# Kernel tuning notes

Hardware: AMD Instinct MI355X
Metric: run time of the kernel (lower is better)

Reference implementation:

```python
import jax, jax.numpy as jnp
import numpy as np

B, S, E, H = 4, 2048, 1024, 16
HD = E // H  # 64 head dim


def setup_inputs() -> dict:
    key = jax.random.key(0)
    ks = jax.random.split(key, 6)
    x = jax.random.normal(ks[0], (B, S, E), dtype=jnp.float32)
    mask = jax.random.randint(ks[1], (B, S, S), 0, 2, dtype=jnp.int32)
    # per-head qkv Linear(E -> 3*HD), stacked over heads: weight [H, 3*HD, E]
    lim = 1.0 / np.sqrt(E)
    Wqkv = jax.random.uniform(ks[2], (H, 3 * HD, E), minval=-lim, maxval=lim, dtype=jnp.float32)
    bqkv = jax.random.uniform(ks[3], (H, 3 * HD), minval=-lim, maxval=lim, dtype=jnp.float32)
    Wo = jax.random.uniform(ks[4], (E, E), minval=-lim, maxval=lim, dtype=jnp.float32)
    bo = jax.random.uniform(ks[5], (E,), minval=-lim, maxval=lim, dtype=jnp.float32)
    return {"x": x, "mask": mask, "Wqkv": Wqkv, "bqkv": bqkv, "Wo": Wo, "bo": bo}


def reference(x, mask, Wqkv, bqkv, Wo, bo):
    # fused per-head qkv projection: [B,S,E] x [H,3HD,E] -> [B,H,S,3HD]
    qkv = jnp.einsum('bse,hfe->bhsf', x, Wqkv) + bqkv[None, :, None, :]
    q, k, v = jnp.split(qkv, 3, axis=-1)  # each [B,H,S,HD]
    scale = 1.0 / jnp.sqrt(jnp.float32(HD))
    scores = jnp.einsum('bhqd,bhkd->bhqk', q, k) * scale  # [B,H,S,S]
    # NOTE: original masked_fill sets masked scores to 0.0 (not -inf)
    scores = jnp.where(mask[:, None, :, :] == 1, 0.0, scores)
    attn = jax.nn.softmax(scores, axis=-1)
    ctx = jnp.einsum('bhqk,bhkd->bhqd', attn, v)  # [B,H,S,HD]
    ctx = ctx.transpose(0, 2, 1, 3).reshape(B, S, E)  # concat heads
    return ctx @ Wo.T + bo
```

## Files before the change

### kernel.cpp

```cpp
#include <hip/hip_runtime.h>
#include <stdint.h>

#define B_ 4
#define S_ 2048
#define E_ 1024
#define H_ 16
#define HD_ 64

typedef __attribute__((ext_vector_type(8))) short bf16x8;
typedef __attribute__((ext_vector_type(4))) float f32x4;

__device__ __forceinline__ ushort f2b(float f) {
    union { float f; uint32_t u; } c; c.f = f;
    return (ushort)((c.u + 0x8000u) >> 16);
}

__device__ __forceinline__ uint32_t pkbf_t(float a, float b) {
    union { float f; uint32_t u; } ca, cb; ca.f = a; cb.f = b;
#if __has_builtin(__builtin_amdgcn_perm)
    return __builtin_amdgcn_perm(cb.u, ca.u, 0x07060302u);
#else
    return (ca.u >> 16) | (cb.u & 0xFFFF0000u);
#endif
}

__device__ __forceinline__ uint32_t keepmask(uint32_t wn, int pos) {
#if __has_builtin(__builtin_amdgcn_sbfe)
    return (uint32_t)__builtin_amdgcn_sbfe((int)wn, pos, 1);
#else
    return (uint32_t)(((int32_t)(wn << (31 - pos))) >> 31);
#endif
}

#if __has_builtin(__builtin_amdgcn_exp2f)
#define EXP2(x) __builtin_amdgcn_exp2f(x)
#else
#define EXP2(x) exp2f(x)
#endif

__device__ __forceinline__ void gl2lds16(const ushort* g, const ushort* l) {
    __builtin_amdgcn_global_load_lds(
        (const __attribute__((address_space(1))) unsigned int*)g,
        (__attribute__((address_space(3))) unsigned int*)l,
        16, 0, 0);
}

__global__ __launch_bounds__(256) void cvt_all(
    const float* __restrict__ x, const float* __restrict__ wq, const float* __restrict__ wo,
    ushort* __restrict__ xb, ushort* __restrict__ wqb, ushort* __restrict__ wob) {
    int i = blockIdx.x * 256 + threadIdx.x;
    const float* src; ushort* dst; int off;
    if (i < 2097152)      { src = x;  dst = xb;  off = i; }
    else if (i < 2883584) { src = wq; dst = wqb; off = i - 2097152; }
    else                  { src = wo; dst = wob; off = i - 2883584; }
    float4 f = ((const float4*)src)[off];
    ushort4 o;
    o.x = f2b(f.x); o.y = f2b(f.y); o.z = f2b(f.z); o.w = f2b(f.w);
    ((ushort4*)dst)[off] = o;
}

__global__ __launch_bounds__(256) void pack_mask(const int* __restrict__ mask,
                                                 uint32_t* __restrict__ mb) {
    int i = blockIdx.x * 256 + threadIdx.x;
    unsigned long long bal = __ballot(mask[i] == 1);
    int lane = threadIdx.x & 63;
    if (lane < 2) {
        int b = i >> 22, q = (i >> 11) & 2047, c = i & 2047;
        int kt = c >> 6;
        mb[((uint64_t)(b * 32 + kt) * 2048 + q) * 2 + lane] =
            (lane == 0) ? (uint32_t)bal : (uint32_t)(bal >> 32);
    }
}

template <int KD>
__device__ __forceinline__ void gemm_bt_core(
    const ushort* __restrict__ A, const ushort* __restrict__ Bm,
    int m0, int n0, ushort* L, f32x4 (&acc)[4][4])
{
    constexpr int NST = KD / 32;
    const int tid  = threadIdx.x;
    const int lane = tid & 63;
    const int wave = tid >> 6;
    const int wm = wave >> 1, wn = wave & 1;
    const int fr = lane & 15;
    const int fk = (lane >> 4) * 8;
    const int lrow = lane >> 2;
    const int lk   = (lane & 3) * 8;

    const f32x4 fz = {0.f, 0.f, 0.f, 0.f};
#pragma unroll
    for (int i = 0; i < 4; ++i)
#pragma unroll
        for (int j = 0; j < 4; ++j) acc[i][j] = fz;

    ushort* s0 = L;
    ushort* s1 = L + 8192;
    ushort* s2 = L + 16384;

    const uint64_t arow = (uint64_t)(m0 + lrow) * KD + lk;
    const uint64_t brow = (uint64_t)(n0 + lrow) * KD + lk;

#define GEMM_STAGE(k0, slot)                                                     \
    {                                                                            \
        _Pragma("unroll")                                                        \
        for (int t = 0; t < 2; ++t) {                                            \
            const int r0 = t * 64 + wave * 16;                                   \
            gl2lds16(&A [arow + (uint64_t)r0 * KD + (k0)], &(slot)[r0 * 32]);    \
            gl2lds16(&Bm[brow + (uint64_t)r0 * KD + (k0)], &(slot)[4096 + r0 * 32]); \
        }                                                                        \
    }

    GEMM_STAGE(0, s0);
    GEMM_STAGE(32, s1);
    asm volatile("s_waitcnt vmcnt(4)" ::: "memory");
    __builtin_amdgcn_s_barrier();
    __builtin_amdgcn_sched_barrier(0);

    ushort* cur = s0; ushort* nxt = s1; ushort* tgt = s2;

    for (int kt = 0; kt < NST; ++kt) {
        if (kt < NST - 2) GEMM_STAGE((kt + 2) * 32, tgt);

        bf16x8 af[4], bfr[4];
#pragma unroll
        for (int i = 0; i < 4; ++i)
            af[i] = *(const bf16x8*)&cur[(wm * 64 + i * 16 + fr) * 32 + fk];
#pragma unroll
        for (int j = 0; j < 4; ++j)
            bfr[j] = *(const bf16x8*)&cur[4096 + (wn * 64 + j * 16 + fr) * 32 + fk];
        __builtin_amdgcn_s_setprio(1);
#pragma unroll
        for (int i = 0; i < 4; ++i)
#pragma unroll
            for (int j = 0; j < 4; ++j)
                acc[i][j] = __builtin_amdgcn_mfma_f32_16x16x32_bf16(af[i], bfr[j], acc[i][j], 0, 0, 0);
        __builtin_amdgcn_s_setprio(0);

        if (kt < NST - 2) {
            asm volatile("s_waitcnt vmcnt(4)" ::: "memory");
        } else {
            asm volatile("s_waitcnt vmcnt(0)" ::: "memory");
        }
        __builtin_amdgcn_s_barrier();
        __builtin_amdgcn_sched_barrier(0);

        ushort* o = cur; cur = nxt; nxt = tgt; tgt = o;
    }
#undef GEMM_STAGE
}

__global__ __launch_bounds__(256) void qkv_gemm(
    const ushort* __restrict__ xb, const ushort* __restrict__ wb,
    const float* __restrict__ bqkv,
    ushort* __restrict__ qo, ushort* __restrict__ ko, ushort* __restrict__ vto)
{
    __shared__ __align__(16) ushort L[24576];
    f32x4 acc[4][4];
    const int lin = blockIdx.x;
    const int swz = (lin & 7) * 192 + (lin >> 3);
    const int m0 = (swz & 63) * 128;
    const int n0 = (swz >> 6) * 128;
    gemm_bt_core<1024>(xb, wb, m0, n0, L, acc);

    const int lane = threadIdx.x & 63, wave = threadIdx.x >> 6;
    const int wm = wave >> 1, wn = wave & 1;
    const int col = lane & 15, rg = lane >> 4;
    const float QSC = 0.125f * 1.4426950408889634f;
#pragma unroll
    for (int j = 0; j < 4; ++j) {
        const int n = n0 + wn * 64 + j * 16 + col;
        const int h = n / 192, f = n % 192;
        const float bias = bqkv[n];
#pragma unroll
        for (int i2 = 0; i2 < 4; ++i2) {
            const int mbase = m0 + wm * 64 + i2 * 16 + rg * 4;
            if (f < 128) {
#pragma unroll
                for (int v = 0; v < 4; ++v) {
                    const int m = mbase + v;
                    const int b = m >> 11, s = m & 2047;
                    const float val = acc[i2][j][v] + bias;
                    if (f < 64) qo[((uint64_t)(b * 16 + h) * 2048 + s) * 64 + f]        = f2b(val * QSC);
                    else        ko[((uint64_t)(b * 16 + h) * 2048 + s) * 64 + (f - 64)] = f2b(val);
                }
            } else {
                const int b = mbase >> 11, s = mbase & 2047;
                ushort4 pk;
                pk.x = f2b(acc[i2][j][0] + bias);
                pk.y = f2b(acc[i2][j][1] + bias);
                pk.z = f2b(acc[i2][j][2] + bias);
                pk.w = f2b(acc[i2][j][3] + bias);
                *(ushort4*)&vto[((uint64_t)(b * 16 + h) * 64 + (f - 128)) * 2048 + s] = pk;
            }
        }
    }
}

__global__ __launch_bounds__(256, 3) void attn_kernel(
    const ushort* __restrict__ qa, const ushort* __restrict__ ka,
    const ushort* __restrict__ vta, const uint32_t* __restrict__ mbits,
    ushort* __restrict__ ctxo)
{
    __shared__ __align__(16) ushort LDSH[24576];
    ushort* const Ks0 = LDSH;
    ushort* const Vt0 = LDSH + 4096;
    ushort* const Ks1 = LDSH + 8192;
    ushort* const Vt1 = LDSH + 12288;
    ushort* const Ks2 = LDSH + 16384;
    ushort* const Vt2 = LDSH + 20480;
    ushort* const CTX = LDSH;

    const int bid = blockIdx.x;
    const int bh = (bid & 7) * 8 + (bid >> 7);
    const int qb = (bid >> 3) & 15;
    const int b = bh >> 4;
    const int tid = threadIdx.x, lane = tid & 63, wave = tid >> 6;
    const int col = lane & 15, rg = lane >> 4;

    const uint64_t bhoff = (uint64_t)bh * (S_ * 64);
    const ushort* qp = qa + bhoff + (uint64_t)qb * 128 * 64;
    const ushort* kp = ka + bhoff;
    const ushort* vp = vta + bhoff;
    const uint32_t* mk0 = mbits + ((uint64_t)(b * 32) * 2048 + qb * 128 + wave * 32 + col) * 2;
    const uint32_t* mk1 = mk0 + 32;

    const int lr = lane >> 3;
    const int usw = (lane & 7) ^ lr;
    const int r0s = wave * 16 + lr;
    const int r1s = r0s + 8;
    const int sg0 = (r0s & 32) | ((r0s & 12) << 1) | ((r0s & 16) >> 2) | (r0s & 3);
    const int sg1 = (r1s & 32) | ((r1s & 12) << 1) | ((r1s & 16) >> 2) | (r1s & 3);
    const int kb0 = sg0 * 64 + usw * 8;
    const int kb1 = sg1 * 64 + usw * 8;
    const int vb0 = r0s * 2048 + usw * 8;
    const int vb1 = r1s * 2048 + usw * 8;
    const int ldst0 = wave * 1024;
    const int ldst1 = ldst0 + 512;

    bf16x8 aq[2][2];
#pragma unroll
    for (int i = 0; i < 2; ++i)
#pragma unroll
        for (int k2 = 0; k2 < 2; ++k2)
            aq[i][k2] = *(const bf16x8*)&qp[(wave * 32 + i * 16 + col) * 64 + k2 * 32 + rg * 8];

    gl2lds16(&kp[kb0], &Ks0[ldst0]);
    gl2lds16(&kp[kb1], &Ks0[ldst1]);
    gl2lds16(&vp[vb0], &Vt0[ldst0]);
    gl2lds16(&vp[vb1], &Vt0[ldst1]);
    uint2 m_cur0 = *(const uint2*)mk0;
    uint2 m_cur1 = *(const uint2*)mk1;
    gl2lds16(&kp[4096 + kb0], &Ks1[ldst0]);
    gl2lds16(&kp[4096 + kb1], &Ks1[ldst1]);
    gl2lds16(&vp[vb0 + 64], &Vt1[ldst0]);
    gl2lds16(&vp[vb1 + 64], &Vt1[ldst1]);
    uint2 m_nxt0 = *(const uint2*)(mk0 + 4096);
    uint2 m_nxt1 = *(const uint2*)(mk1 + 4096);
    uint2 m_new0 = m_nxt0, m_new1 = m_nxt1;
    asm volatile("s_waitcnt vmcnt(0)" ::: "memory");
    __builtin_amdgcn_s_barrier();
    __builtin_amdgcn_sched_barrier(0);

    const f32x4 fz = {0.f, 0.f, 0.f, 0.f};
    f32x4 acc[4][2];
#pragma unroll
    for (int dt = 0; dt < 4; ++dt)
#pragma unroll
        for (int i = 0; i < 2; ++i) acc[dt][i] = fz;
    f32x4 acc5[2] = {fz, fz};

    bf16x8 vone;
#pragma unroll
    for (int e = 0; e < 8; ++e) vone[e] = (short)0x3F80;

    int bpos[2][4];
#pragma unroll
    for (int p = 0; p < 2; ++p)
#pragma unroll
        for (int v = 0; v < 4; ++v) bpos[p][v] = rg * 8 + p * 4 + v;

    const int u0 = (rg ^ (col & 7)) << 3;

    const ushort* cK = Ks0; const ushort* cV = Vt0;
    const ushort* nK = Ks1; const ushort* nV = Vt1;
    ushort* tK = Ks2; ushort* tV = Vt2;

    for (int kt = 0; kt < 32; ++kt) {
        if (kt < 30) {
            const int k2 = (kt + 2) * 4096;
            gl2lds16(&kp[k2 + kb0], &tK[ldst0]);
            gl2lds16(&kp[k2 + kb1], &tK[ldst1]);
            gl2lds16(&vp[vb0 + (kt + 2) * 64], &tV[ldst0]);
            gl2lds16(&vp[vb1 + (kt + 2) * 64], &tV[ldst1]);
            m_new0 = *(const uint2*)(mk0 + (uint64_t)(kt + 2) * 4096);
            m_new1 = *(const uint2*)(mk1 + (uint64_t)(kt + 2) * 4096);
        }

        f32x4 sc[2][4];
        __builtin_amdgcn_s_setprio(1);
#pragma unroll
        for (int j = 0; j < 4; ++j) {
            bf16x8 bk0 = *(const bf16x8*)&cK[(j * 16 + col) * 64 + u0];
            bf16x8 bk1 = *(const bf16x8*)&cK[(j * 16 + col) * 64 + (u0 ^ 32)];
#pragma unroll
            for (int i = 0; i < 2; ++i) {
                f32x4 z = __builtin_amdgcn_mfma_f32_16x16x32_bf16(bk0, aq[i][0], fz, 0, 0, 0);
                sc[i][j] = __builtin_amdgcn_mfma_f32_16x16x32_bf16(bk1, aq[i][1], z, 0, 0, 0);
            }
        }
        __builtin_amdgcn_s_setprio(0);

        bf16x8 bp[2][2];
#pragma unroll
        for (int i = 0; i < 2; ++i) {
            const uint2 mw = i ? m_cur1 : m_cur0;
            const uint32_t wnx = ~mw.x, wny = ~mw.y;
            union { uint32_t w[4]; bf16x8 v; } p0, p1;
#pragma unroll
            for (int j = 0; j < 4; ++j) {
                const uint32_t wn = (j & 2) ? wny : wnx;
                const int p = j & 1;
                float pe[4];
#pragma unroll
                for (int v = 0; v < 4; ++v) {
                    union { float f; uint32_t u; } cu;
                    cu.f = sc[i][j][v];
                    cu.u &= keepmask(wn, bpos[p][v]);
                    pe[v] = EXP2(cu.f);
                }
                const uint32_t lo = pkbf_t(pe[0], pe[1]);
                const uint32_t hi = pkbf_t(pe[2], pe[3]);
                if (j < 2) { p0.w[p * 2] = lo; p0.w[p * 2 + 1] = hi; }
                else       { p1.w[p * 2] = lo; p1.w[p * 2 + 1] = hi; }
            }
            bp[i][0] = p0.v;
            bp[i][1] = p1.v;
        }

        __builtin_amdgcn_s_setprio(1);
#pragma unroll
        for (int i = 0; i < 2; ++i) {
            acc5[i] = __builtin_amdgcn_mfma_f32_16x16x32_bf16(vone, bp[i][0], acc5[i], 0, 0, 0);
            acc5[i] = __builtin_amdgcn_mfma_f32_16x16x32_bf16(vone, bp[i][1], acc5[i], 0, 0, 0);
        }
#pragma unroll
        for (int dt = 0; dt < 4; ++dt) {
            bf16x8 av0 = *(const bf16x8*)&cV[(dt * 16 + col) * 64 + u0];
            bf16x8 av1 = *(const bf16x8*)&cV[(dt * 16 + col) * 64 + (u0 ^ 32)];
#pragma unroll
            for (int i = 0; i < 2; ++i) {
                acc[dt][i] = __builtin_amdgcn_mfma_f32_16x16x32_bf16(av0, bp[i][0], acc[dt][i], 0, 0, 0);
                acc[dt][i] = __builtin_amdgcn_mfma_f32_16x16x32_bf16(av1, bp[i][1], acc[dt][i], 0, 0, 0);
            }
        }
        __builtin_amdgcn_s_setprio(0);

        if (kt < 30) {
            asm volatile("s_waitcnt vmcnt(6)" ::: "memory");
        } else {
            asm volatile("s_waitcnt vmcnt(0)" ::: "memory");
        }
        __builtin_amdgcn_s_barrier();
        __builtin_amdgcn_sched_barrier(0);

        const ushort* oK = cK; const ushort* oV = cV;
        cK = nK; cV = nV; nK = tK; nV = tV; tK = (ushort*)oK; tV = (ushort*)oV;
        m_cur0 = m_nxt0; m_cur1 = m_nxt1; m_nxt0 = m_new0; m_nxt1 = m_new1;
    }

    float linv[2];
#pragma unroll
    for (int i = 0; i < 2; ++i) linv[i] = 1.0f / acc5[i][0];

#pragma unroll
    for (int dt = 0; dt < 4; ++dt)
#pragma unroll
        for (int i = 0; i < 2; ++i) {
            const int q = wave * 32 + i * 16 + col;
            const int d = dt * 16 + rg * 4;
            const int gg = (d >> 3) ^ (q & 7);
            ushort4 pk;
            pk.x = f2b(acc[dt][i][0] * linv[i]);
            pk.y = f2b(acc[dt][i][1] * linv[i]);
            pk.z = f2b(acc[dt][i][2] * linv[i]);
            pk.w = f2b(acc[dt][i][3] * linv[i]);
            *(ushort4*)&CTX[q * 64 + gg * 8 + (d & 7)] = pk;
        }
    __syncthreads();
    const int h = bh & 15;
    const uint64_t obase = (uint64_t)(b * S_ + qb * 128) * E_ + (uint64_t)h * 64;
#pragma unroll
    for (int t4 = 0; t4 < 4; ++t4) {
        const int id = tid + t4 * 256;
        const int r = id >> 3, c8 = id & 7;
        *(bf16x8*)&ctxo[obase + (uint64_t)r * E_ + c8 * 8] =
            *(const bf16x8*)&CTX[r * 64 + ((c8 ^ (r & 7)) << 3)];
    }
}

__global__ __launch_bounds__(256) void out_gemm(
    const ushort* __restrict__ ctxb, const ushort* __restrict__ wob,
    const float* __restrict__ bo, float* __restrict__ out)
{
    __shared__ __align__(16) ushort L[24576];
    f32x4 acc[4][4];
    const int lin = blockIdx.x;
    const int swz = (lin & 7) * 64 + (lin >> 3);
    const int m0 = (swz & 63) * 128;
    const int n0 = (swz >> 6) * 128;
    gemm_bt_core<1024>(ctxb, wob, m0, n0, L, acc);

    const int lane = threadIdx.x & 63, wave = threadIdx.x >> 6;
    const int wm = wave >> 1, wn = wave & 1;
    const int col = lane & 15, rg = lane >> 4;
#pragma unroll
    for (int j = 0; j < 4; ++j) {
        const int n = n0 + wn * 64 + j * 16 + col;
        const float bias = bo[n];
#pragma unroll
        for (int i2 = 0; i2 < 4; ++i2) {
            const int mb2 = m0 + wm * 64 + i2 * 16 + rg * 4;
#pragma unroll
            for (int v = 0; v < 4; ++v)
                out[(uint64_t)(mb2 + v) * 1024 + n] = acc[i2][j][v] + bias;
        }
    }
}

extern "C" void kernel_launch(void* const* d_in, const int* in_sizes, int n_in,
                              void* d_out, int out_size, void* d_ws, size_t ws_size,
                              hipStream_t stream)
{
    const float* x    = (const float*)d_in[0];
    const int*   mask = (const int*)d_in[1];
    const float* Wqkv = (const float*)d_in[2];
    const float* bqkv = (const float*)d_in[3];
    const float* Wo   = (const float*)d_in[4];
    const float* bo   = (const float*)d_in[5];
    float* out = (float*)d_out;

    char* p = (char*)d_ws;
    ushort* xb  = (ushort*)p; p += (size_t)8388608 * 2;
    ushort* wqb = (ushort*)p; p += (size_t)3145728 * 2;
    ushort* wob = (ushort*)p; p += (size_t)1048576 * 2;
    ushort* qo  = (ushort*)p; p += (size_t)8388608 * 2;
    ushort* ko  = (ushort*)p; p += (size_t)8388608 * 2;
    ushort* vto = (ushort*)p; p += (size_t)8388608 * 2;
    ushort* ctx = (ushort*)p; p += (size_t)8388608 * 2;
    uint32_t* mb = (uint32_t*)p;

    cvt_all<<<12288, 256, 0, stream>>>(x, Wqkv, Wo, xb, wqb, wob);
    pack_mask<<<65536, 256, 0, stream>>>(mask, mb);
    qkv_gemm<<<1536, 256, 0, stream>>>(xb, wqb, bqkv, qo, ko, vto);
    attn_kernel<<<1024, 256, 0, stream>>>(qo, ko, vto, mb, ctx);
    out_gemm<<<512, 256, 0, stream>>>(ctx, wob, bo, out);
}
```

Before: 353.3 us.

## Software-pipeline attention loop: overlap QK^T of next tile with softmax/PV

Restructures the attention inner loop so each phase computes QK^T scores for tile kt while running the mask/exp softmax and PV MFMAs for tile kt-1, using ping-pong score registers and a manual two-step unroll. The K/V tile issue moves after a barrier that follows the PV step, and the mask words are carried in a four-deep register rotation. The aim is to hide exp/VALU latency behind MFMA work and keep the matrix units busy. In exchange it raises register pressure, since two score sets are live at once, and adds an extra barrier per iteration.

```diff
diff --git a/kernel.cpp b/kernel.cpp
--- a/kernel.cpp
+++ b/kernel.cpp
@@ -244,19 +244,19 @@
         for (int k2 = 0; k2 < 2; ++k2)
             aq[i][k2] = *(const bf16x8*)&qp[(wave * 32 + i * 16 + col) * 64 + k2 * 32 + rg * 8];
 
+    uint2 m_a0 = *(const uint2*)mk0;
+    uint2 m_a1 = *(const uint2*)mk1;
+    uint2 m_b0 = *(const uint2*)(mk0 + 4096);
+    uint2 m_b1 = *(const uint2*)(mk1 + 4096);
+    uint2 m_c0, m_c1, m_d0, m_d1;
     gl2lds16(&kp[kb0], &Ks0[ldst0]);
     gl2lds16(&kp[kb1], &Ks0[ldst1]);
     gl2lds16(&vp[vb0], &Vt0[ldst0]);
     gl2lds16(&vp[vb1], &Vt0[ldst1]);
-    uint2 m_cur0 = *(const uint2*)mk0;
-    uint2 m_cur1 = *(const uint2*)mk1;
     gl2lds16(&kp[4096 + kb0], &Ks1[ldst0]);
     gl2lds16(&kp[4096 + kb1], &Ks1[ldst1]);
     gl2lds16(&vp[vb0 + 64], &Vt1[ldst0]);
     gl2lds16(&vp[vb1 + 64], &Vt1[ldst1]);
-    uint2 m_nxt0 = *(const uint2*)(mk0 + 4096);
-    uint2 m_nxt1 = *(const uint2*)(mk1 + 4096);
-    uint2 m_new0 = m_nxt0, m_new1 = m_nxt1;
     asm volatile("s_waitcnt vmcnt(0)" ::: "memory");
     __builtin_amdgcn_s_barrier();
     __builtin_amdgcn_sched_barrier(0);
@@ -281,92 +281,125 @@
 
     const int u0 = (rg ^ (col & 7)) << 3;
 
-    const ushort* cK = Ks0; const ushort* cV = Vt0;
-    const ushort* nK = Ks1; const ushort* nV = Vt1;
-    ushort* tK = Ks2; ushort* tV = Vt2;
-
-    for (int kt = 0; kt < 32; ++kt) {
-        if (kt < 30) {
-            const int k2 = (kt + 2) * 4096;
-            gl2lds16(&kp[k2 + kb0], &tK[ldst0]);
-            gl2lds16(&kp[k2 + kb1], &tK[ldst1]);
-            gl2lds16(&vp[vb0 + (kt + 2) * 64], &tV[ldst0]);
-            gl2lds16(&vp[vb1 + (kt + 2) * 64], &tV[ldst1]);
-            m_new0 = *(const uint2*)(mk0 + (uint64_t)(kt + 2) * 4096);
-            m_new1 = *(const uint2*)(mk1 + (uint64_t)(kt + 2) * 4096);
-        }
-
-        f32x4 sc[2][4];
-        __builtin_amdgcn_s_setprio(1);
-#pragma unroll
-        for (int j = 0; j < 4; ++j) {
-            bf16x8 bk0 = *(const bf16x8*)&cK[(j * 16 + col) * 64 + u0];
-            bf16x8 bk1 = *(const bf16x8*)&cK[(j * 16 + col) * 64 + (u0 ^ 32)];
-#pragma unroll
-            for (int i = 0; i < 2; ++i) {
-                f32x4 z = __builtin_amdgcn_mfma_f32_16x16x32_bf16(bk0, aq[i][0], fz, 0, 0, 0);
-                sc[i][j] = __builtin_amdgcn_mfma_f32_16x16x32_bf16(bk1, aq[i][1], z, 0, 0, 0);
-            }
-        }
-        __builtin_amdgcn_s_setprio(0);
-
-        bf16x8 bp[2][2];
-#pragma unroll
-        for (int i = 0; i < 2; ++i) {
-            const uint2 mw = i ? m_cur1 : m_cur0;
-            const uint32_t wnx = ~mw.x, wny = ~mw.y;
-            union { uint32_t w[4]; bf16x8 v; } p0, p1;
-#pragma unroll
-            for (int j = 0; j < 4; ++j) {
-                const uint32_t wn = (j & 2) ? wny : wnx;
-                const int p = j & 1;
-                float pe[4];
-#pragma unroll
-                for (int v = 0; v < 4; ++v) {
-                    union { float f; uint32_t u; } cu;
-                    cu.f = sc[i][j][v];
-                    cu.u &= keepmask(wn, bpos[p][v]);
-                    pe[v] = EXP2(cu.f);
-                }
-                const uint32_t lo = pkbf_t(pe[0], pe[1]);
-                const uint32_t hi = pkbf_t(pe[2], pe[3]);
-                if (j < 2) { p0.w[p * 2] = lo; p0.w[p * 2 + 1] = hi; }
-                else       { p1.w[p * 2] = lo; p1.w[p * 2 + 1] = hi; }
-            }
-            bp[i][0] = p0.v;
-            bp[i][1] = p1.v;
-        }
-
-        __builtin_amdgcn_s_setprio(1);
-#pragma unroll
-        for (int i = 0; i < 2; ++i) {
-            acc5[i] = __builtin_amdgcn_mfma_f32_16x16x32_bf16(vone, bp[i][0], acc5[i], 0, 0, 0);
-            acc5[i] = __builtin_amdgcn_mfma_f32_16x16x32_bf16(vone, bp[i][1], acc5[i], 0, 0, 0);
-        }
-#pragma unroll
-        for (int dt = 0; dt < 4; ++dt) {
-            bf16x8 av0 = *(const bf16x8*)&cV[(dt * 16 + col) * 64 + u0];
-            bf16x8 av1 = *(const bf16x8*)&cV[(dt * 16 + col) * 64 + (u0 ^ 32)];
-#pragma unroll
-            for (int i = 0; i < 2; ++i) {
-                acc[dt][i] = __builtin_amdgcn_mfma_f32_16x16x32_bf16(av0, bp[i][0], acc[dt][i], 0, 0, 0);
-                acc[dt][i] = __builtin_amdgcn_mfma_f32_16x16x32_bf16(av1, bp[i][1], acc[dt][i], 0, 0, 0);
-            }
-        }
-        __builtin_amdgcn_s_setprio(0);
-
-        if (kt < 30) {
-            asm volatile("s_waitcnt vmcnt(6)" ::: "memory");
-        } else {
-            asm volatile("s_waitcnt vmcnt(0)" ::: "memory");
-        }
-        __builtin_amdgcn_s_barrier();
-        __builtin_amdgcn_sched_barrier(0);
-
-        const ushort* oK = cK; const ushort* oV = cV;
-        cK = nK; cV = nV; nK = tK; nV = tV; tK = (ushort*)oK; tV = (ushort*)oV;
-        m_cur0 = m_nxt0; m_cur1 = m_nxt1; m_nxt0 = m_new0; m_nxt1 = m_new1;
-    }
+    f32x4 scA[2][4], scB[2][4];
+    bf16x8 bp[2][2];
+
+#define QKT_STEP(PK, SCOUT)                                                    \
+    _Pragma("unroll")                                                          \
+    for (int j = 0; j < 4; ++j) {                                              \
+        bf16x8 bk0 = *(const bf16x8*)&(PK)[(j * 16 + col) * 64 + u0];          \
+        bf16x8 bk1 = *(const bf16x8*)&(PK)[(j * 16 + col) * 64 + (u0 ^ 32)];   \
+        _Pragma("unroll")                                                      \
+        for (int i = 0; i < 2; ++i) {                                          \
+            f32x4 z = __builtin_amdgcn_mfma_f32_16x16x32_bf16(bk0, aq[i][0], fz, 0, 0, 0); \
+            SCOUT[i][j] = __builtin_amdgcn_mfma_f32_16x16x32_bf16(bk1, aq[i][1], z, 0, 0, 0); \
+        }                                                                      \
+    }
+
+#define SOFTMAX_STEP(SCIN)                                                     \
+    _Pragma("unroll")                                                          \
+    for (int i = 0; i < 2; ++i) {                                              \
+        const uint2 mw = i ? m_a1 : m_a0;                                      \
+        const uint32_t wnx = ~mw.x, wny = ~mw.y;                               \
+        union { uint32_t w[4]; bf16x8 v; } p0, p1;                             \
+        _Pragma("unroll")                                                      \
+        for (int j = 0; j < 4; ++j) {                                          \
+            const uint32_t wn = (j & 2) ? wny : wnx;                           \
+            const int p = j & 1;                                               \
+            float pe[4];                                                       \
+            _Pragma("unroll")                                                  \
+            for (int v = 0; v < 4; ++v) {                                      \
+                union { float f; uint32_t u; } cu;                             \
+                cu.f = SCIN[i][j][v];                                          \
+                cu.u &= keepmask(wn, bpos[p][v]);                              \
+                pe[v] = EXP2(cu.f);                                            \
+            }                                                                  \
+            const uint32_t lo = pkbf_t(pe[0], pe[1]);                          \
+            const uint32_t hi = pkbf_t(pe[2], pe[3]);                          \
+            if (j < 2) { p0.w[p * 2] = lo; p0.w[p * 2 + 1] = hi; }             \
+            else       { p1.w[p * 2] = lo; p1.w[p * 2 + 1] = hi; }             \
+        }                                                                      \
+        bp[i][0] = p0.v;                                                       \
+        bp[i][1] = p1.v;                                                       \
+    }
+
+#define PV_STEP(PVP)                                                           \
+    _Pragma("unroll")                                                          \
+    for (int i = 0; i < 2; ++i) {                                              \
+        acc5[i] = __builtin_amdgcn_mfma_f32_16x16x32_bf16(vone, bp[i][0], acc5[i], 0, 0, 0); \
+        acc5[i] = __builtin_amdgcn_mfma_f32_16x16x32_bf16(vone, bp[i][1], acc5[i], 0, 0, 0); \
+    }                                                                          \
+    _Pragma("unroll")                                                          \
+    for (int dt = 0; dt < 4; ++dt) {                                           \
+        bf16x8 av0 = *(const bf16x8*)&(PVP)[(dt * 16 + col) * 64 + u0];        \
+        bf16x8 av1 = *(const bf16x8*)&(PVP)[(dt * 16 + col) * 64 + (u0 ^ 32)]; \
+        _Pragma("unroll")                                                      \
+        for (int i = 0; i < 2; ++i) {                                          \
+            acc[dt][i] = __builtin_amdgcn_mfma_f32_16x16x32_bf16(av0, bp[i][0], acc[dt][i], 0, 0, 0); \
+            acc[dt][i] = __builtin_amdgcn_mfma_f32_16x16x32_bf16(av1, bp[i][1], acc[dt][i], 0, 0, 0); \
+        }                                                                      \
+    }
+
+    m_c0 = *(const uint2*)(mk0 + (uint64_t)2 * 4096);
+    m_c1 = *(const uint2*)(mk1 + (uint64_t)2 * 4096);
+    gl2lds16(&kp[2 * 4096 + kb0], &Ks2[ldst0]);
+    gl2lds16(&kp[2 * 4096 + kb1], &Ks2[ldst1]);
+    gl2lds16(&vp[vb0 + 2 * 64], &Vt2[ldst0]);
+    gl2lds16(&vp[vb1 + 2 * 64], &Vt2[ldst1]);
+    QKT_STEP(Ks0, scA)
+    asm volatile("s_waitcnt vmcnt(4)" ::: "memory");
+    __builtin_amdgcn_s_barrier();
+    __builtin_amdgcn_sched_barrier(0);
+
+    ushort* pKA = Ks1; ushort* pKB = Ks2; ushort* pKC = Ks0;
+    ushort* pVA = Vt1; ushort* pVB = Vt2; ushort* pVC = Vt0;
+
+#define ATTN_PHASE(KT, SCIN, SCOUT)                                            \
+    {                                                                          \
+        const int kt_ = (KT);                                                  \
+        if (kt_ <= 29) {                                                       \
+            m_d0 = *(const uint2*)(mk0 + (uint64_t)(kt_ + 2) * 4096);          \
+            m_d1 = *(const uint2*)(mk1 + (uint64_t)(kt_ + 2) * 4096);          \
+        }                                                                      \
+        __builtin_amdgcn_s_setprio(1);                                         \
+        QKT_STEP(pKA, SCOUT)                                                   \
+        __builtin_amdgcn_s_setprio(0);                                         \
+        SOFTMAX_STEP(SCIN)                                                     \
+        __builtin_amdgcn_s_setprio(1);                                         \
+        PV_STEP(pVC)                                                           \
+        __builtin_amdgcn_s_setprio(0);                                         \
+        __builtin_amdgcn_s_barrier();       \
+        if (kt_ <= 29) {                                                       \
+            const int ko_ = (kt_ + 2) * 4096;                                  \
+            gl2lds16(&kp[ko_ + kb0], &pKC[ldst0]);                             \
+            gl2lds16(&kp[ko_ + kb1], &pKC[ldst1]);                             \
+            gl2lds16(&vp[vb0 + (kt_ + 2) * 64], &pVC[ldst0]);                  \
+            gl2lds16(&vp[vb1 + (kt_ + 2) * 64], &pVC[ldst1]);                  \
+            asm volatile("s_waitcnt vmcnt(4)" ::: "memory");                   \
+        } else {                                                               \
+            asm volatile("s_waitcnt vmcnt(0)" ::: "memory");                   \
+        }                                                                      \
+        __builtin_amdgcn_s_barrier();                                          \
+        __builtin_amdgcn_sched_barrier(0);                                     \
+        m_a0 = m_b0; m_a1 = m_b1; m_b0 = m_c0; m_b1 = m_c1;                    \
+        m_c0 = m_d0; m_c1 = m_d1;                                              \
+        { ushort* t_ = pKA; pKA = pKB; pKB = pKC; pKC = t_; }                  \
+        { ushort* t_ = pVA; pVA = pVB; pVB = pVC; pVC = t_; }                  \
+    }
+
+    for (int k2 = 0; k2 < 15; ++k2) {
+        ATTN_PHASE(2 * k2 + 1, scA, scB)
+        ATTN_PHASE(2 * k2 + 2, scB, scA)
+    }
+    ATTN_PHASE(31, scA, scB)
+
+    SOFTMAX_STEP(scB)
+    PV_STEP(pVC)
+
+#undef ATTN_PHASE
+#undef QKT_STEP
+#undef SOFTMAX_STEP
+#undef PV_STEP
 
     float linv[2];
 #pragma unroll
```

New measurement: 421.4 us. +19.3%, slower.
